# Optimization experiments

Hardware: AMD Instinct MI355X
Metric: run time of the kernel (lower is better)

## Reference

```python
import jax, jax.numpy as jnp
import numpy as np

C = 256
CQ = max(1, C // 8)  # 32


def setup_inputs() -> dict:
    key = jax.random.key(0)
    ks = jax.random.split(key, 8)
    B, D, H, W = 4, 16, 16, 16
    x = jax.random.normal(ks[0], (B, C, D, H, W), dtype=jnp.float32)
    # 1x1 Conv3d == channel-wise linear; weights scaled ~1/sqrt(C) for stable softmax
    s = 0.05
    wq = jax.random.normal(ks[1], (CQ, C), dtype=jnp.float32) * s
    bq = jax.random.normal(ks[2], (CQ,), dtype=jnp.float32) * s
    wk = jax.random.normal(ks[3], (CQ, C), dtype=jnp.float32) * s
    bk = jax.random.normal(ks[4], (CQ,), dtype=jnp.float32) * s
    wv = jax.random.normal(ks[5], (C, C), dtype=jnp.float32) * s
    bv = jax.random.normal(ks[6], (C,), dtype=jnp.float32) * s
    gamma = jax.random.normal(ks[7], (1,), dtype=jnp.float32)
    return {"x": x, "wq": wq, "bq": bq, "wk": wk, "bk": bk,
            "wv": wv, "bv": bv, "gamma": gamma}


def reference(x, wq, bq, wk, bk, wv, bv, gamma):
    B, Cc, D, H, W = x.shape
    N = D * H * W
    xf = x.reshape(B, Cc, N)                                   # [B,C,N]
    # 1x1 conv projections (channel contractions)
    q = jnp.einsum('qc,bcn->bnq', wq, xf) + bq                 # [B,N,Cq]
    k = jnp.einsum('qc,bcn->bqn', wk, xf) + bk[None, :, None]  # [B,Cq,N]
    v = jnp.einsum('oc,bcn->bon', wv, xf) + bv[None, :, None]  # [B,C,N]
    att = jax.nn.softmax(jnp.einsum('bnq,bqm->bnm', q, k), axis=-1)  # [B,N,N]
    out = jnp.einsum('bom,bnm->bon', v, att)                   # [B,C,N]
    out = gamma[0] * out + xf
    return out.reshape(B, Cc, D, H, W)
```

## Files before the change

### kernel.cpp

```cpp
#include <hip/hip_runtime.h>
#include <stdint.h>

typedef unsigned short u16;
typedef unsigned int u32;
typedef short s16x8 __attribute__((ext_vector_type(8)));
typedef float f32x4 __attribute__((ext_vector_type(4)));
typedef float f32x16 __attribute__((ext_vector_type(16)));

#define LOG2E 1.44269504088896340736f
#define FIXMAX 40.0f

__device__ __forceinline__ u16 f2bf(float f) {
    union { float f; u32 i; } c; c.f = f;
    u32 u = c.i + 0x7FFFu + ((c.i >> 16) & 1u);
    return (u16)(u >> 16);
}
__device__ __forceinline__ float fast_exp2(float x) {
#if __has_builtin(__builtin_amdgcn_exp2f)
    return __builtin_amdgcn_exp2f(x);
#else
    return exp2f(x);
#endif
}
__device__ __forceinline__ u32 cvtpk_bf16(float lo, float hi) {
    u32 r;
    asm("v_cvt_pk_bf16_f32 %0, %1, %2" : "=v"(r) : "v"(lo), "v"(hi));
    return r;
}
__device__ __forceinline__ void swap32(u32 a, u32 b, u32& x, u32& y, int half) {
#if __has_builtin(__builtin_amdgcn_permlane32_swap)
    auto r = __builtin_amdgcn_permlane32_swap(a, b, false, false);
    x = r[0]; y = r[1];
#else
    u32 ax = (u32)__shfl_xor((int)a, 32, 64);
    u32 bx = (u32)__shfl_xor((int)b, 32, 64);
    x = half ? bx : a;
    y = half ? b : ax;
#endif
}


__global__ __launch_bounds__(256) void convert_w(
    const float* __restrict__ wq, const float* __restrict__ wk,
    const float* __restrict__ wv, u16* __restrict__ wsb)
{
    int i = blockIdx.x * 256 + threadIdx.x;
    float v;
    if (i < 65536)      v = wv[i];
    else if (i < 73728) v = wq[i - 65536];
    else                v = wk[i - 73728];
    wsb[i] = f2bf(v);
}

__global__ __launch_bounds__(256, 2) void proj_kernel(
    const float* __restrict__ x,
    const u16* __restrict__ wq_bf, const float* __restrict__ bq,
    const u16* __restrict__ wk_bf, const float* __restrict__ bk,
    const u16* __restrict__ wv_bf, const float* __restrict__ bv,
    u16* __restrict__ q_ws, u16* __restrict__ k_ws, u16* __restrict__ v_ws)
{
    __shared__ u16 XT[32 * 264];
    const int t  = threadIdx.x;
    const int b  = blockIdx.x >> 7;
    const int n0 = (blockIdx.x & 127) << 5;

    {
        const int c2 = t & 127;
        const int nh = (t >> 7) << 4;
        size_t base0 = (size_t)(b * 256 + 2 * c2) * 4096 + n0 + nh;
        float4 R0[4], R1[4];
        #pragma unroll
        for (int g = 0; g < 4; ++g) {
            R0[g] = *(const float4*)(x + base0 + 4 * g);
            R1[g] = *(const float4*)(x + base0 + 4096 + 4 * g);
        }
        u32* lds32 = (u32*)XT;
        #pragma unroll
        for (int g = 0; g < 4; ++g) {
            const float* p0 = (const float*)&R0[g];
            const float* p1 = (const float*)&R1[g];
            #pragma unroll
            for (int e = 0; e < 4; ++e) {
                int nl = nh + g * 4 + e;
                lds32[nl * 132 + c2] = (u32)f2bf(p0[e]) | ((u32)f2bf(p1[e]) << 16);
            }
        }
    }
    __syncthreads();

    const int wave = t >> 6, lane = t & 63, quad = lane >> 4, l15 = lane & 15;
    const int orow = wave * 64;

    f32x4 accV[4][2];
    f32x4 accQK[2];
    #pragma unroll
    for (int i = 0; i < 4; ++i) { accV[i][0] = (f32x4)0.0f; accV[i][1] = (f32x4)0.0f; }
    accQK[0] = (f32x4)0.0f; accQK[1] = (f32x4)0.0f;

    const int qsel = wave >> 1;
    const u16* wsel = qsel ? wk_bf : wq_bf;
    const int qc = ((wave & 1) << 4) + l15;

    #pragma unroll
    for (int co = 0; co < 8; ++co) {
        int cb = co * 32 + quad * 8;
        s16x8 X0 = *(const s16x8*)(XT + l15 * 264 + cb);
        s16x8 X1 = *(const s16x8*)(XT + (16 + l15) * 264 + cb);
        s16x8 WV[4];
        #pragma unroll
        for (int rt = 0; rt < 4; ++rt)
            WV[rt] = *(const s16x8*)(wv_bf + (size_t)(orow + rt * 16 + l15) * 256 + cb);
        s16x8 WQK = *(const s16x8*)(wsel + (size_t)qc * 256 + cb);

        #pragma unroll
        for (int rt = 0; rt < 4; ++rt) {
            accV[rt][0] = __builtin_amdgcn_mfma_f32_16x16x32_bf16(WV[rt], X0, accV[rt][0], 0, 0, 0);
            accV[rt][1] = __builtin_amdgcn_mfma_f32_16x16x32_bf16(WV[rt], X1, accV[rt][1], 0, 0, 0);
        }
        accQK[0] = __builtin_amdgcn_mfma_f32_16x16x32_bf16(X0, WQK, accQK[0], 0, 0, 0);
        accQK[1] = __builtin_amdgcn_mfma_f32_16x16x32_bf16(X1, WQK, accQK[1], 0, 0, 0);
    }

    {
        const int mh = (l15 >> 3) & 1;
        const int j  = l15 & 7;
        #pragma unroll
        for (int rt = 0; rt < 4; ++rt) {
            int ob = orow + rt * 16 + quad * 4;
            float bvf[4];
            #pragma unroll
            for (int r = 0; r < 4; ++r) bvf[r] = bv[ob + r];
            #pragma unroll
            for (int ct = 0; ct < 2; ++ct) {
                int kt = ((n0 + ct * 16) >> 4);
                #pragma unroll
                for (int r = 0; r < 4; ++r) {
                    int o = ob + r;
                    size_t addr = ((((size_t)(b * 8 + (o >> 5)) * 256) + kt) << 9)
                                + (size_t)((mh << 5) + (o & 31)) * 8 + j;
                    v_ws[addr] = f2bf(accV[rt][ct][r] + bvf[r]);
                }
            }
        }
    }
    if (qsel == 0) {
        float bias = bq[qc];
        #pragma unroll
        for (int r = 0; r < 2; ++r)
            #pragma unroll
            for (int reg = 0; reg < 4; ++reg) {
                int n = n0 + r * 16 + quad * 4 + reg;
                q_ws[(size_t)(b * 4096 + n) * 32 + qc] = f2bf((accQK[r][reg] + bias) * LOG2E);
            }
    } else {
        float bias = bk[qc];
        const int ckt = qc >> 4, ch2 = (qc >> 3) & 1, cj = qc & 7;
        #pragma unroll
        for (int r = 0; r < 2; ++r)
            #pragma unroll
            for (int reg = 0; reg < 4; ++reg) {
                int m = n0 + r * 16 + quad * 4 + reg;
                size_t addr = ((((size_t)(b * 128 + (m >> 5)) * 2) + ckt) << 9)
                            + (size_t)((ch2 << 5) + (m & 31)) * 8 + cj;
                k_ws[addr] = f2bf(accQK[r][reg] + bias);
            }
    }
}

__global__ __launch_bounds__(512, 2) void attn_kernel(
    const u16* __restrict__ q_ws, const u16* __restrict__ k_ws, const u16* __restrict__ v_ws,
    const float* __restrict__ x, const float* __restrict__ gamma_p, float* __restrict__ out)
{
    __shared__ float Ored[2][256 * 32];
    __shared__ float l_sh[2][4][64];

    const int t = threadIdx.x;
    const int wave = t >> 6, lane = t & 63;
    const int nh = wave & 1;
    const int ms = wave >> 1;
    const int half = lane >> 5, n31 = lane & 31;

    const int bid = blockIdx.x;
    const int xcd = bid & 7;
    const int b   = xcd >> 1;
    const int nt  = ((xcd & 1) << 5) | (bid >> 3);
    const int n0  = nt << 6;
    const int nw  = n0 + (nh << 5);

    const u16* qrow = q_ws + ((size_t)(b * 4096 + nw + n31) << 5) + half * 8;
    const s16x8 QF0 = *(const s16x8*)(qrow);
    const s16x8 QF1 = *(const s16x8*)(qrow + 16);

    const u16* kfb = k_ws + (((size_t)b * 256) << 9);
    const u16* vfb = v_ws + (((size_t)b * 8 * 256) << 9);

    f32x16 accO[8];
    #pragma unroll
    for (int ot = 0; ot < 8; ++ot) accO[ot] = (f32x16)0.0f;
    float l_acc = 0.0f;

    for (int ch = 0; ch < 32; ++ch) {
        const int mt  = (ms << 5) + ch;
        const int ktb = mt << 1;

        const u16* kp = kfb + (((size_t)mt * 2) << 9) + lane * 8;
        s16x8 KF0 = *(const s16x8*)(kp);
        s16x8 KF1 = *(const s16x8*)(kp + 512);
        f32x16 st = (f32x16)0.0f;
        st = __builtin_amdgcn_mfma_f32_32x32x16_bf16(KF0, QF0, st, 0, 0, 0);
        st = __builtin_amdgcn_mfma_f32_32x32x16_bf16(KF1, QF1, st, 0, 0, 0);

        float p[16];
        #pragma unroll
        for (int r = 0; r < 16; ++r) p[r] = fast_exp2(st[r] - FIXMAX);
        {
            float t0 = (p[0] + p[1]) + (p[2] + p[3]);
            float t1 = (p[4] + p[5]) + (p[6] + p[7]);
            float t2 = (p[8] + p[9]) + (p[10] + p[11]);
            float t3 = (p[12] + p[13]) + (p[14] + p[15]);
            l_acc += (t0 + t1) + (t2 + t3);
        }

        u32 A0 = cvtpk_bf16(p[0],  p[1]),  A1 = cvtpk_bf16(p[2],  p[3]);
        u32 B0 = cvtpk_bf16(p[4],  p[5]),  B1 = cvtpk_bf16(p[6],  p[7]);
        u32 C0 = cvtpk_bf16(p[8],  p[9]),  C1 = cvtpk_bf16(p[10], p[11]);
        u32 D0 = cvtpk_bf16(p[12], p[13]), D1 = cvtpk_bf16(p[14], p[15]);
        u32 w0, w1, w2, w3, y0, y1, y2, y3;
        swap32(A0, B0, w0, w2, half);
        swap32(A1, B1, w1, w3, half);
        swap32(C0, D0, y0, y2, half);
        swap32(C1, D1, y1, y3, half);
        union { u32 w[4]; s16x8 v; } PB0, PB1;
        PB0.w[0] = w0; PB0.w[1] = w1; PB0.w[2] = w2; PB0.w[3] = w3;
        PB1.w[0] = y0; PB1.w[1] = y1; PB1.w[2] = y2; PB1.w[3] = y3;

        const u16* vp = vfb + (((size_t)ktb * 64 + lane) << 3);
        #pragma unroll
        for (int ot = 0; ot < 8; ++ot) {
            s16x8 V0 = *(const s16x8*)(vp);
            s16x8 V1 = *(const s16x8*)(vp + 512);
            accO[ot] = __builtin_amdgcn_mfma_f32_32x32x16_bf16(V0, PB0.v, accO[ot], 0, 0, 0);
            accO[ot] = __builtin_amdgcn_mfma_f32_32x32x16_bf16(V1, PB1.v, accO[ot], 0, 0, 0);
            vp += (size_t)256 * 512;
        }
    }

    l_sh[nh][ms][lane] = l_acc;
    float* Od = Ored[nh];
    if (ms == 0) {
        #pragma unroll
        for (int ot = 0; ot < 8; ++ot)
            #pragma unroll
            for (int r = 0; r < 16; ++r) {
                const int o = (ot << 5) + (r & 3) + ((r >> 2) << 3) + (half << 2);
                Od[(o << 5) + n31] = accO[ot][r];
            }
    }
    __syncthreads();
    #pragma unroll
    for (int s = 1; s < 4; ++s) {
        if (ms == s) {
            #pragma unroll
            for (int ot = 0; ot < 8; ++ot)
                #pragma unroll
                for (int r = 0; r < 16; ++r) {
                    const int o = (ot << 5) + (r & 3) + ((r >> 2) << 3) + (half << 2);
                    Od[(o << 5) + n31] += accO[ot][r];
                }
        }
        __syncthreads();
    }

    const float gamma = gamma_p[0];
    const int tn  = t & 31;
    const int tnh = (t >> 5) & 1;
    const int og  = t >> 6;
    float lt = 0.0f;
    #pragma unroll
    for (int s = 0; s < 4; ++s) lt += l_sh[tnh][s][tn] + l_sh[tnh][s][32 + tn];
    const float rinv = gamma / lt;
    const int n = n0 + (tnh << 5) + tn;
    const float* OdR = Ored[tnh];
    #pragma unroll
    for (int i = 0; i < 32; ++i) {
        const int o = og + (i << 3);
        const size_t idx = ((size_t)(b * 256 + o) << 12) + n;
        out[idx] = OdR[(o << 5) + tn] * rinv + x[idx];
    }
}

extern "C" void kernel_launch(void* const* d_in, const int* in_sizes, int n_in,
                              void* d_out, int out_size, void* d_ws, size_t ws_size,
                              hipStream_t stream) {
    const float* x  = (const float*)d_in[0];
    const float* wq = (const float*)d_in[1];
    const float* bq = (const float*)d_in[2];
    const float* wk = (const float*)d_in[3];
    const float* bk = (const float*)d_in[4];
    const float* wv = (const float*)d_in[5];
    const float* bv = (const float*)d_in[6];
    const float* gm = (const float*)d_in[7];

    u16* wsb   = (u16*)d_ws;
    u16* wv_bf = wsb;
    u16* wq_bf = wsb + 65536;
    u16* wk_bf = wsb + 73728;
    u16* q_ws  = wsb + 81920;
    u16* k_ws  = q_ws + 4 * 4096 * 32;
    u16* v_ws  = k_ws + 4 * 4096 * 32;

    convert_w<<<320, 256, 0, stream>>>(wq, wk, wv, wsb);
    proj_kernel<<<512, 256, 0, stream>>>(x, wq_bf, bq, wk_bf, bk, wv_bf, bv, q_ws, k_ws, v_ws);
    attn_kernel<<<256, 512, 0, stream>>>(q_ws, k_ws, v_ws, x, gm, (float*)d_out);
}
```

Baseline: 148.6 us.

## Prefetch K and V fragments, stagger warp start chunks, raise MFMA priority

Measured after the change: 153.1 us. 3.0% more time.

```diff
diff --git a/kernel.cpp b/kernel.cpp
--- a/kernel.cpp
+++ b/kernel.cpp
@@ -199,16 +199,45 @@
     for (int ot = 0; ot < 8; ++ot) accO[ot] = (f32x16)0.0f;
     float l_acc = 0.0f;
 
-    for (int ch = 0; ch < 32; ++ch) {
-        const int mt  = (ms << 5) + ch;
-        const int ktb = mt << 1;
-
-        const u16* kp = kfb + (((size_t)mt * 2) << 9) + lane * 8;
-        s16x8 KF0 = *(const s16x8*)(kp);
-        s16x8 KF1 = *(const s16x8*)(kp + 512);
+#if __has_builtin(__builtin_amdgcn_s_sleep)
+    if (ms == 1)      __builtin_amdgcn_s_sleep(3);
+    else if (ms == 2) __builtin_amdgcn_s_sleep(6);
+    else if (ms == 3) __builtin_amdgcn_s_sleep(9);
+#endif
+
+    const int chBase = ms << 3;
+
+    {
+        const int mt0 = (ms << 5) + chBase;
+        const u16* kp0 = kfb + ((size_t)mt0 << 10) + lane * 8;
+    }
+    const int mt0 = (ms << 5) + chBase;
+    const u16* kp0 = kfb + ((size_t)mt0 << 10) + lane * 8;
+    s16x8 KF0 = *(const s16x8*)(kp0);
+    s16x8 KF1 = *(const s16x8*)(kp0 + 512);
+
+    for (int it = 0; it < 32; ++it) {
+        const int ch  = (it + chBase) & 31;
+        const int chn = (it + 1 + chBase) & 31;
+        const int mtc = (ms << 5) + ch;
+        const int ktb = mtc << 1;
+
+        const u16* vp0 = vfb + (((size_t)ktb * 64 + lane) << 3);
+        s16x8 V0[8];
+        #pragma unroll
+        for (int ot = 0; ot < 8; ++ot)
+            V0[ot] = *(const s16x8*)(vp0 + (size_t)ot * 131072);
+
         f32x16 st = (f32x16)0.0f;
         st = __builtin_amdgcn_mfma_f32_32x32x16_bf16(KF0, QF0, st, 0, 0, 0);
         st = __builtin_amdgcn_mfma_f32_32x32x16_bf16(KF1, QF1, st, 0, 0, 0);
+
+        {
+            const int mtn = (ms << 5) + chn;
+            const u16* kpn = kfb + ((size_t)mtn << 10) + lane * 8;
+            KF0 = *(const s16x8*)(kpn);
+            KF1 = *(const s16x8*)(kpn + 512);
+        }
 
         float p[16];
         #pragma unroll
@@ -234,15 +263,19 @@
         PB0.w[0] = w0; PB0.w[1] = w1; PB0.w[2] = w2; PB0.w[3] = w3;
         PB1.w[0] = y0; PB1.w[1] = y1; PB1.w[2] = y2; PB1.w[3] = y3;
 
-        const u16* vp = vfb + (((size_t)ktb * 64 + lane) << 3);
-        #pragma unroll
-        for (int ot = 0; ot < 8; ++ot) {
-            s16x8 V0 = *(const s16x8*)(vp);
-            s16x8 V1 = *(const s16x8*)(vp + 512);
-            accO[ot] = __builtin_amdgcn_mfma_f32_32x32x16_bf16(V0, PB0.v, accO[ot], 0, 0, 0);
-            accO[ot] = __builtin_amdgcn_mfma_f32_32x32x16_bf16(V1, PB1.v, accO[ot], 0, 0, 0);
-            vp += (size_t)256 * 512;
-        }
+        s16x8 V1[8];
+        #pragma unroll
+        for (int ot = 0; ot < 8; ++ot)
+            V1[ot] = *(const s16x8*)(vp0 + 512 + (size_t)ot * 131072);
+
+        __builtin_amdgcn_s_setprio(1);
+        #pragma unroll
+        for (int ot = 0; ot < 8; ++ot)
+            accO[ot] = __builtin_amdgcn_mfma_f32_32x32x16_bf16(V0[ot], PB0.v, accO[ot], 0, 0, 0);
+        #pragma unroll
+        for (int ot = 0; ot < 8; ++ot)
+            accO[ot] = __builtin_amdgcn_mfma_f32_32x32x16_bf16(V1[ot], PB1.v, accO[ot], 0, 0, 0);
+        __builtin_amdgcn_s_setprio(0);
     }
 
     l_sh[nh][ms][lane] = l_acc;
```

## Split attention waves by output channels and reuse V fragments across query tiles

Applied to the files above, without the earlier changes.

Result: no change. 145.9 us (-1.8%).

```diff
diff --git a/kernel.cpp b/kernel.cpp
--- a/kernel.cpp
+++ b/kernel.cpp
@@ -136,7 +136,7 @@
                 #pragma unroll
                 for (int r = 0; r < 4; ++r) {
                     int o = ob + r;
-                    size_t addr = ((((size_t)(b * 8 + (o >> 5)) * 256) + kt) << 9)
+                    size_t addr = ((((size_t)(b * 256 + kt) * 8) + (o >> 5)) << 9)
                                 + (size_t)((mh << 5) + (o & 31)) * 8 + j;
                     v_ws[addr] = f2bf(accV[rt][ct][r] + bvf[r]);
                 }
@@ -171,13 +171,13 @@
     const u16* __restrict__ q_ws, const u16* __restrict__ k_ws, const u16* __restrict__ v_ws,
     const float* __restrict__ x, const float* __restrict__ gamma_p, float* __restrict__ out)
 {
-    __shared__ float Ored[2][256 * 32];
-    __shared__ float l_sh[2][4][64];
+    __shared__ float Ored[256 * 64];
+    __shared__ float l_sh[4][2][64];
 
     const int t = threadIdx.x;
     const int wave = t >> 6, lane = t & 63;
-    const int nh = wave & 1;
-    const int ms = wave >> 1;
+    const int og = wave >> 2;
+    const int ms = wave & 3;
     const int half = lane >> 5, n31 = lane & 31;
 
     const int bid = blockIdx.x;
@@ -185,107 +185,143 @@
     const int b   = xcd >> 1;
     const int nt  = ((xcd & 1) << 5) | (bid >> 3);
     const int n0  = nt << 6;
-    const int nw  = n0 + (nh << 5);
-
-    const u16* qrow = q_ws + ((size_t)(b * 4096 + nw + n31) << 5) + half * 8;
-    const s16x8 QF0 = *(const s16x8*)(qrow);
-    const s16x8 QF1 = *(const s16x8*)(qrow + 16);
+
+    const u16* qrow0 = q_ws + ((size_t)(b * 4096 + n0 + n31) << 5) + half * 8;
+    const s16x8 QA0 = *(const s16x8*)(qrow0);
+    const s16x8 QA1 = *(const s16x8*)(qrow0 + 16);
+    const s16x8 QB0 = *(const s16x8*)(qrow0 + 1024);
+    const s16x8 QB1 = *(const s16x8*)(qrow0 + 1024 + 16);
 
     const u16* kfb = k_ws + (((size_t)b * 256) << 9);
-    const u16* vfb = v_ws + (((size_t)b * 8 * 256) << 9);
-
-    f32x16 accO[8];
-    #pragma unroll
-    for (int ot = 0; ot < 8; ++ot) accO[ot] = (f32x16)0.0f;
-    float l_acc = 0.0f;
+    const u16* vfb = v_ws + ((size_t)b << 20);
+
+    f32x16 accO[4][2];
+    #pragma unroll
+    for (int ot = 0; ot < 4; ++ot) { accO[ot][0] = (f32x16)0.0f; accO[ot][1] = (f32x16)0.0f; }
+    float l0_acc = 0.0f, l1_acc = 0.0f;
 
     for (int ch = 0; ch < 32; ++ch) {
         const int mt  = (ms << 5) + ch;
         const int ktb = mt << 1;
 
-        const u16* kp = kfb + (((size_t)mt * 2) << 9) + lane * 8;
+        const u16* kp = kfb + ((size_t)mt << 10) + lane * 8;
         s16x8 KF0 = *(const s16x8*)(kp);
         s16x8 KF1 = *(const s16x8*)(kp + 512);
-        f32x16 st = (f32x16)0.0f;
-        st = __builtin_amdgcn_mfma_f32_32x32x16_bf16(KF0, QF0, st, 0, 0, 0);
-        st = __builtin_amdgcn_mfma_f32_32x32x16_bf16(KF1, QF1, st, 0, 0, 0);
-
-        float p[16];
-        #pragma unroll
-        for (int r = 0; r < 16; ++r) p[r] = fast_exp2(st[r] - FIXMAX);
+
+        const u16* vp = vfb + (((size_t)(ktb * 8 + og * 4)) << 9) + lane * 8;
+        s16x8 V0[4], V1[4];
+        #pragma unroll
+        for (int ot = 0; ot < 4; ++ot) {
+            V0[ot] = *(const s16x8*)(vp + ot * 512);
+            V1[ot] = *(const s16x8*)(vp + 4096 + ot * 512);
+        }
+
+        f32x16 st0 = (f32x16)0.0f, st1 = (f32x16)0.0f;
+        st0 = __builtin_amdgcn_mfma_f32_32x32x16_bf16(KF0, QA0, st0, 0, 0, 0);
+        st0 = __builtin_amdgcn_mfma_f32_32x32x16_bf16(KF1, QA1, st0, 0, 0, 0);
+        st1 = __builtin_amdgcn_mfma_f32_32x32x16_bf16(KF0, QB0, st1, 0, 0, 0);
+        st1 = __builtin_amdgcn_mfma_f32_32x32x16_bf16(KF1, QB1, st1, 0, 0, 0);
+
+        float p0[16], p1[16];
+        #pragma unroll
+        for (int r = 0; r < 16; ++r) p0[r] = fast_exp2(st0[r] - FIXMAX);
+        #pragma unroll
+        for (int r = 0; r < 16; ++r) p1[r] = fast_exp2(st1[r] - FIXMAX);
+        if (og == 0) {
+            float a0 = (p0[0] + p0[1]) + (p0[2] + p0[3]);
+            float a1 = (p0[4] + p0[5]) + (p0[6] + p0[7]);
+            float a2 = (p0[8] + p0[9]) + (p0[10] + p0[11]);
+            float a3 = (p0[12] + p0[13]) + (p0[14] + p0[15]);
+            l0_acc += (a0 + a1) + (a2 + a3);
+            float b0 = (p1[0] + p1[1]) + (p1[2] + p1[3]);
+            float b1 = (p1[4] + p1[5]) + (p1[6] + p1[7]);
+            float b2 = (p1[8] + p1[9]) + (p1[10] + p1[11]);
+            float b3 = (p1[12] + p1[13]) + (p1[14] + p1[15]);
+            l1_acc += (b0 + b1) + (b2 + b3);
+        }
+
+        union { u32 w[4]; s16x8 v; } P0B0, P0B1, P1B0, P1B1;
         {
-            float t0 = (p[0] + p[1]) + (p[2] + p[3]);
-            float t1 = (p[4] + p[5]) + (p[6] + p[7]);
-            float t2 = (p[8] + p[9]) + (p[10] + p[11]);
-            float t3 = (p[12] + p[13]) + (p[14] + p[15]);
-            l_acc += (t0 + t1) + (t2 + t3);
-        }
-
-        u32 A0 = cvtpk_bf16(p[0],  p[1]),  A1 = cvtpk_bf16(p[2],  p[3]);
-        u32 B0 = cvtpk_bf16(p[4],  p[5]),  B1 = cvtpk_bf16(p[6],  p[7]);
-        u32 C0 = cvtpk_bf16(p[8],  p[9]),  C1 = cvtpk_bf16(p[10], p[11]);
-        u32 D0 = cvtpk_bf16(p[12], p[13]), D1 = cvtpk_bf16(p[14], p[15]);
-        u32 w0, w1, w2, w3, y0, y1, y2, y3;
-        swap32(A0, B0, w0, w2, half);
-        swap32(A1, B1, w1, w3, half);
-        swap32(C0, D0, y0, y2, half);
-        swap32(C1, D1, y1, y3, half);
-        union { u32 w[4]; s16x8 v; } PB0, PB1;
-        PB0.w[0] = w0; PB0.w[1] = w1; PB0.w[2] = w2; PB0.w[3] = w3;
-        PB1.w[0] = y0; PB1.w[1] = y1; PB1.w[2] = y2; PB1.w[3] = y3;
-
-        const u16* vp = vfb + (((size_t)ktb * 64 + lane) << 3);
-        #pragma unroll
-        for (int ot = 0; ot < 8; ++ot) {
-            s16x8 V0 = *(const s16x8*)(vp);
-            s16x8 V1 = *(const s16x8*)(vp + 512);
-            accO[ot] = __builtin_amdgcn_mfma_f32_32x32x16_bf16(V0, PB0.v, accO[ot], 0, 0, 0);
-            accO[ot] = __builtin_amdgcn_mfma_f32_32x32x16_bf16(V1, PB1.v, accO[ot], 0, 0, 0);
-            vp += (size_t)256 * 512;
-        }
-    }
-
-    l_sh[nh][ms][lane] = l_acc;
-    float* Od = Ored[nh];
+            u32 A0 = cvtpk_bf16(p0[0],  p0[1]),  A1 = cvtpk_bf16(p0[2],  p0[3]);
+            u32 B0 = cvtpk_bf16(p0[4],  p0[5]),  B1 = cvtpk_bf16(p0[6],  p0[7]);
+            u32 C0 = cvtpk_bf16(p0[8],  p0[9]),  C1 = cvtpk_bf16(p0[10], p0[11]);
+            u32 D0 = cvtpk_bf16(p0[12], p0[13]), D1 = cvtpk_bf16(p0[14], p0[15]);
+            u32 w0, w1, w2, w3, y0, y1, y2, y3;
+            swap32(A0, B0, w0, w2, half);
+            swap32(A1, B1, w1, w3, half);
+            swap32(C0, D0, y0, y2, half);
+            swap32(C1, D1, y1, y3, half);
+            P0B0.w[0] = w0; P0B0.w[1] = w1; P0B0.w[2] = w2; P0B0.w[3] = w3;
+            P0B1.w[0] = y0; P0B1.w[1] = y1; P0B1.w[2] = y2; P0B1.w[3] = y3;
+        }
+        {
+            u32 A0 = cvtpk_bf16(p1[0],  p1[1]),  A1 = cvtpk_bf16(p1[2],  p1[3]);
+            u32 B0 = cvtpk_bf16(p1[4],  p1[5]),  B1 = cvtpk_bf16(p1[6],  p1[7]);
+            u32 C0 = cvtpk_bf16(p1[8],  p1[9]),  C1 = cvtpk_bf16(p1[10], p1[11]);
+            u32 D0 = cvtpk_bf16(p1[12], p1[13]), D1 = cvtpk_bf16(p1[14], p1[15]);
+            u32 w0, w1, w2, w3, y0, y1, y2, y3;
+            swap32(A0, B0, w0, w2, half);
+            swap32(A1, B1, w1, w3, half);
+            swap32(C0, D0, y0, y2, half);
+            swap32(C1, D1, y1, y3, half);
+            P1B0.w[0] = w0; P1B0.w[1] = w1; P1B0.w[2] = w2; P1B0.w[3] = w3;
+            P1B1.w[0] = y0; P1B1.w[1] = y1; P1B1.w[2] = y2; P1B1.w[3] = y3;
+        }
+
+        #pragma unroll
+        for (int ot = 0; ot < 4; ++ot) {
+            accO[ot][0] = __builtin_amdgcn_mfma_f32_32x32x16_bf16(V0[ot], P0B0.v, accO[ot][0], 0, 0, 0);
+            accO[ot][0] = __builtin_amdgcn_mfma_f32_32x32x16_bf16(V1[ot], P0B1.v, accO[ot][0], 0, 0, 0);
+            accO[ot][1] = __builtin_amdgcn_mfma_f32_32x32x16_bf16(V0[ot], P1B0.v, accO[ot][1], 0, 0, 0);
+            accO[ot][1] = __builtin_amdgcn_mfma_f32_32x32x16_bf16(V1[ot], P1B1.v, accO[ot][1], 0, 0, 0);
+        }
+    }
+
+    if (og == 0) {
+        l_sh[ms][half][n31]      = l0_acc;
+        l_sh[ms][half][32 + n31] = l1_acc;
+    }
     if (ms == 0) {
         #pragma unroll
-        for (int ot = 0; ot < 8; ++ot)
-            #pragma unroll
-            for (int r = 0; r < 16; ++r) {
-                const int o = (ot << 5) + (r & 3) + ((r >> 2) << 3) + (half << 2);
-                Od[(o << 5) + n31] = accO[ot][r];
-            }
+        for (int ot = 0; ot < 4; ++ot)
+            #pragma unroll
+            for (int nhh = 0; nhh < 2; ++nhh)
+                #pragma unroll
+                for (int r = 0; r < 16; ++r) {
+                    const int o = (og << 7) + (ot << 5) + (r & 3) + ((r >> 2) << 3) + (half << 2);
+                    Ored[(o << 6) + (nhh << 5) + n31] = accO[ot][nhh][r];
+                }
     }
     __syncthreads();
     #pragma unroll
     for (int s = 1; s < 4; ++s) {
         if (ms == s) {
             #pragma unroll
-            for (int ot = 0; ot < 8; ++ot)
+            for (int ot = 0; ot < 4; ++ot)
                 #pragma unroll
-                for (int r = 0; r < 16; ++r) {
-                    const int o = (ot << 5) + (r & 3) + ((r >> 2) << 3) + (half << 2);
-                    Od[(o << 5) + n31] += accO[ot][r];
-                }
+                for (int nhh = 0; nhh < 2; ++nhh)
+                    #pragma unroll
+                    for (int r = 0; r < 16; ++r) {
+                        const int o = (og << 7) + (ot << 5) + (r & 3) + ((r >> 2) << 3) + (half << 2);
+                        Ored[(o << 6) + (nhh << 5) + n31] += accO[ot][nhh][r];
+                    }
         }
         __syncthreads();
     }
 
     const float gamma = gamma_p[0];
-    const int tn  = t & 31;
-    const int tnh = (t >> 5) & 1;
-    const int og  = t >> 6;
+    const int nn = t & 63;
+    const int oo = t >> 6;
     float lt = 0.0f;
     #pragma unroll
-    for (int s = 0; s < 4; ++s) lt += l_sh[tnh][s][tn] + l_sh[tnh][s][32 + tn];
+    for (int s = 0; s < 4; ++s) lt += l_sh[s][0][nn] + l_sh[s][1][nn];
     const float rinv = gamma / lt;
-    const int n = n0 + (tnh << 5) + tn;
-    const float* OdR = Ored[tnh];
+    const int n = n0 + nn;
     #pragma unroll
     for (int i = 0; i < 32; ++i) {
-        const int o = og + (i << 3);
+        const int o = oo + (i << 3);
         const size_t idx = ((size_t)(b * 256 + o) << 12) + n;
-        out[idx] = OdR[(o << 5) + tn] * rinv + x[idx];
+        out[idx] = Ored[(o << 6) + nn] * rinv + x[idx];
     }
 }
 
```
